# Kernel optimization log

Measured on AMD Instinct MI355X. Metric: run time of the kernel, lower is better.

The kernel has to match this reference:

```python
import jax, jax.numpy as jnp
import numpy as np

B, G, P, H = 32, 5000, 5000, 64
N = B * G
E_CO, E_GG = 1600000, 100000

def _bn(x, g, b):
    # BatchNorm1d in training mode: biased batch stats, eps=1e-5
    m = x.mean(0); v = x.var(0)
    return g * (x - m) * jax.lax.rsqrt(v + 1e-5) + b

def _renorm(t):
    # nn.Embedding(max_norm=True) -> rows renormed to L2 norm <= 1
    n = jnp.linalg.norm(t, axis=1, keepdims=True)
    return t * jnp.minimum(1.0, 1.0 / jnp.maximum(n, 1e-12))

def _sgconv(x, src, dst, w, W, b):
    # SGConv(K=1): gcn_norm (self-loops w=1, symmetric deg norm) spmm, then Linear
    n = x.shape[0]
    sl = jnp.arange(n)
    s = jnp.concatenate([src, sl]); d = jnp.concatenate([dst, sl])
    ww = jnp.concatenate([w, jnp.ones((n,), x.dtype)])
    deg = jax.ops.segment_sum(ww, d, num_segments=n)
    dinv = jnp.where(deg > 0, jax.lax.rsqrt(deg), 0.0)
    coef = dinv[s] * ww * dinv[d]
    agg = jax.ops.segment_sum(coef[:, None] * x[s], d, num_segments=n)
    return agg @ W.T + b

def _mlp3(x, W, b, g, bt):
    # MLP([h,h,h]): Lin-BN-ReLU-Lin-BN (trailing ReLU stripped by [:-1])
    h = jax.nn.relu(_bn(x @ W[0].T + b[0], g[0], bt[0]))
    return _bn(h @ W[1].T + b[1], g[1], bt[1])

def _gears(x, pert_idx, ei_co, w_co, ei_go, w_go, ei_bg, w_bg,
           gene_tab, pos_tab, go_tab, bg_tab, bn_g, bn_b, sg_W, sg_b,
           mlp_W, mlp_b, mlp_g, mlp_bt,
           rec_W1, rec_b1, rec_g1, rec_bt1, rec_W2, rec_b2, rec_g2, rec_bt2,
           indv_w1, indv_b1,
           cg_W1, cg_b1, cg_g1, cg_bt1, cg_W2, cg_b2, cg_g2, cg_bt2,
           indv_w2, indv_b2):
    nb = pert_idx.shape[0]
    ng = gene_tab.shape[0]
    emb = jnp.tile(_renorm(gene_tab), (nb, 1))                     # [B*G,H]
    base = jax.nn.relu(_bn(emb, bn_g[0], bn_b[0]))                 # bn_emb + emb_trans
    pos = jnp.tile(_renorm(pos_tab), (nb, 1))
    pos = _sgconv(pos, ei_co[0], ei_co[1], w_co, sg_W[0], sg_b[0]) # 1 gene-pos GNN layer, no trailing relu
    base = base + 0.2 * pos
    base = _mlp3(base, mlp_W[1], mlp_b[1], mlp_g[1], mlp_bt[1])    # emb_trans_v2
    pgo = _sgconv(_renorm(go_tab), ei_go[0], ei_go[1], w_go, sg_W[1], sg_b[1])
    pbg = _sgconv(_renorm(bg_tab), ei_bg[0], ei_bg[1], w_bg, sg_W[2], sg_b[2])
    pglob = _mlp3(pgo + pbg, mlp_W[0], mlp_b[0], mlp_g[0], mlp_bt[0])  # pert_emb_comb_trans
    base = base.reshape(nb, ng, -1)
    # one valid pert per graph -> pert_track reduces to a gather; pert_fuse then broadcast-add
    emb_total = _mlp3(pglob[pert_idx], mlp_W[2], mlp_b[2], mlp_g[2], mlp_bt[2])  # [B,H]
    base = base + emb_total[:, None, :]
    base = base.reshape(nb * ng, -1)
    base = jax.nn.relu(_bn(base, bn_g[1], bn_b[1]))                # bn_pert_base + transform
    h = jax.nn.relu(_bn(base @ rec_W1.T + rec_b1, rec_g1, rec_bt1))
    out = _bn(h @ rec_W2.T + rec_b2, rec_g2, rec_bt2).reshape(nb, ng, -1)
    w1 = jnp.einsum('bgh,gh->bg', out, indv_w1) + indv_b1          # per-gene decoder 1
    cg = jax.nn.relu(_bn(w1 @ cg_W1.T + cg_b1, cg_g1, cg_bt1))
    cg = _bn(cg @ cg_W2.T + cg_b2, cg_g2, cg_bt2)                  # cross_gene_state [B,H]
    cat = jnp.concatenate([w1[..., None], jnp.broadcast_to(cg[:, None, :], (nb, ng, cg.shape[-1]))], -1)
    out2 = jnp.einsum('bgk,gk->bg', cat, indv_w2) + indv_b2        # per-gene decoder 2
    return out2 + x.reshape(nb, ng)

def setup_inputs():
    ks = jax.random.split(jax.random.key(0), 48)
    rn = lambda i, sh, s=0.05: jax.random.normal(ks[i], sh, jnp.float32) * s
    return {
        "x": rn(0, (N,), 1.0),
        "pert_idx": jax.random.randint(ks[1], (B,), 0, P),
        "ei_co": jax.random.randint(ks[2], (2, E_CO), 0, N),
        "w_co": jax.random.uniform(ks[3], (E_CO,), jnp.float32),
        "ei_go": jax.random.randint(ks[4], (2, E_GG), 0, P),
        "w_go": jax.random.uniform(ks[5], (E_GG,), jnp.float32),
        "ei_bg": jax.random.randint(ks[6], (2, E_GG), 0, P),
        "w_bg": jax.random.uniform(ks[7], (E_GG,), jnp.float32),
        "gene_tab": rn(8, (G, H), 1.0),
        "pos_tab": rn(9, (G, H), 1.0),
        "go_tab": rn(10, (P, H), 1.0),
        "bg_tab": rn(11, (P, H), 1.0),
        "bn_g": jnp.ones((2, H)), "bn_b": jnp.zeros((2, H)),
        "sg_W": rn(12, (3, H, H)), "sg_b": jnp.zeros((3, H)),
        "mlp_W": rn(13, (3, 2, H, H)), "mlp_b": jnp.zeros((3, 2, H)),
        "mlp_g": jnp.ones((3, 2, H)), "mlp_bt": jnp.zeros((3, 2, H)),
        "rec_W1": rn(14, (2 * H, H)), "rec_b1": jnp.zeros((2 * H,)),
        "rec_g1": jnp.ones((2 * H,)), "rec_bt1": jnp.zeros((2 * H,)),
        "rec_W2": rn(15, (H, 2 * H)), "rec_b2": jnp.zeros((H,)),
        "rec_g2": jnp.ones((H,)), "rec_bt2": jnp.zeros((H,)),
        "indv_w1": rn(16, (G, H)), "indv_b1": rn(17, (G,)),
        "cg_W1": rn(18, (H, G), 0.01), "cg_b1": jnp.zeros((H,)),
        "cg_g1": jnp.ones((H,)), "cg_bt1": jnp.zeros((H,)),
        "cg_W2": rn(19, (H, H)), "cg_b2": jnp.zeros((H,)),
        "cg_g2": jnp.ones((H,)), "cg_bt2": jnp.zeros((H,)),
        "indv_w2": rn(20, (G, H + 1)), "indv_b2": rn(21, (G,)),
    }

def reference(x, pert_idx, ei_co, w_co, ei_go, w_go, ei_bg, w_bg,
              gene_tab, pos_tab, go_tab, bg_tab, bn_g, bn_b, sg_W, sg_b,
              mlp_W, mlp_b, mlp_g, mlp_bt,
              rec_W1, rec_b1, rec_g1, rec_bt1, rec_W2, rec_b2, rec_g2, rec_bt2,
              indv_w1, indv_b1,
              cg_W1, cg_b1, cg_g1, cg_bt1, cg_W2, cg_b2, cg_g2, cg_bt2,
              indv_w2, indv_b2):
    return _gears(x, pert_idx, ei_co, w_co, ei_go, w_go, ei_bg, w_bg,
                  gene_tab, pos_tab, go_tab, bg_tab, bn_g, bn_b, sg_W, sg_b,
                  mlp_W, mlp_b, mlp_g, mlp_bt,
                  rec_W1, rec_b1, rec_g1, rec_bt1, rec_W2, rec_b2, rec_g2, rec_bt2,
                  indv_w1, indv_b1,
                  cg_W1, cg_b1, cg_g1, cg_bt1, cg_W2, cg_b2, cg_g2, cg_bt2,
                  indv_w2, indv_b2)
```

## Files before the change

### kernel.cpp

```cpp
#include <hip/hip_runtime.h>

typedef unsigned int u32;
typedef unsigned short u16;

constexpr int Gn  = 5000;
constexpr int Bn  = 32;
constexpr int Pn  = 5000;
constexpr int Nn  = Bn * Gn;
constexpr int ECO = 1600000;
constexpr int EGG = 100000;
constexpr int NTILES = Nn / 128;
constexpr int PTILES = 40;
constexpr int NBK = 625;
constexpr int EPB2 = ECO / 256;

constexpr int oS2 = 128;
constexpr int oZERO = 1536;
constexpr int oA1 = 2048, oB1 = 2112, oA2 = 2176, oB2 = 2240;
constexpr int oA4 = 2304, oB4 = 2432;
constexpr int oA5 = 2560, oB5 = 2624;
constexpr int oAG = 2688, oBG = 2752;
constexpr int oAP1 = 2816, oBP1 = 2880, oAP2 = 2944, oBP2 = 3008;
constexpr int oAvec = 3072, oCvec = 3136, oCcP = 3200;
constexpr int oM  = 4096, oM1 = 8192;
constexpr int oE2 = 16384, oEMB = 18432, oCGRAW = 20480, oCG2 = 22528;
constexpr int oRG  = 24576;
constexpr int oRP  = oRG  + Gn * 64;
constexpr int oQ   = oRP  + Gn * 64;
constexpr int oRGO = oQ   + Gn * 64;
constexpr int oRBG = oRGO + Pn * 64;
constexpr int oAGO = oRBG + Pn * 64;
constexpr int oABG = oAGO + Pn * 64;
constexpr int oM1B = oABG + Pn * 64;
constexpr int oM2B = oM1B + Pn * 64;
constexpr int oDGO = oM2B + Pn * 64;
constexpr int oDBG = oDGO + Pn;
constexpr int oDEG = oDBG + Pn;
constexpr int oW1  = oDEG + Nn;
constexpr int oBUF0 = oW1 + Nn;
constexpr int oBUF1 = oBUF0 + Nn * 64;
constexpr size_t WS_FLOATS = (size_t)oBUF1 + (size_t)Nn * 64;

__device__ inline u16 f2bf(float f) {
  u32 u = __float_as_uint(f);
  u = (u + 0x7fffu + ((u >> 16) & 1u)) >> 16;
  return (u16)u;
}
__device__ inline float bflo(u32 v) { return __uint_as_float(v << 16); }
__device__ inline float bfhi(u32 v) { return __uint_as_float(v & 0xffff0000u); }
__device__ inline float bf2f(u16 v) { return __uint_as_float((u32)v << 16); }

typedef __attribute__((ext_vector_type(8))) short short8v;
typedef __attribute__((ext_vector_type(4))) float f32x4;

__global__ __launch_bounds__(256) void kzero(float* p, int n) {
  int i = blockIdx.x * 256 + threadIdx.x;
  if (i < n) p[i] = 0.f;
}

__global__ __launch_bounds__(256) void krenorm(const float* __restrict__ in, float* __restrict__ out,
                                               float* __restrict__ partial, u16* __restrict__ outb, int rows) {
  int lane = threadIdx.x & 63, wv = threadIdx.x >> 6;
  int gw = blockIdx.x * 4 + wv, nw = gridDim.x * 4;
  float ps = 0.f, pq = 0.f;
  for (int r = gw; r < rows; r += nw) {
    float v = in[r * 64 + lane];
    float sq = v * v;
    for (int off = 32; off; off >>= 1) sq += __shfl_xor(sq, off, 64);
    float nn = sqrtf(sq);
    float s = fminf(1.f, 1.f / fmaxf(nn, 1e-12f));
    float o = v * s;
    out[r * 64 + lane] = o;
    if (outb) outb[r * 64 + lane] = f2bf(o);
    ps += o; pq += o * o;
  }
  if (!partial) return;
  __shared__ float red[4][64], red2[4][64];
  red[wv][lane] = ps; red2[wv][lane] = pq;
  __syncthreads();
  if (wv == 0) {
    float s = red[0][lane] + red[1][lane] + red[2][lane] + red[3][lane];
    float q = red2[0][lane] + red2[1][lane] + red2[2][lane] + red2[3][lane];
    partial[blockIdx.x * 128 + lane] = s;
    partial[blockIdx.x * 128 + 64 + lane] = q;
  }
}

__global__ __launch_bounds__(1024) void kredfin(const float* __restrict__ part, int nblk, int outc,
                                                const float* __restrict__ g, const float* __restrict__ bt,
                                                float* __restrict__ a, float* __restrict__ b,
                                                float* __restrict__ outSQ, float invn) {
  __shared__ float rs[16][64], rq[16][64];
  int t = threadIdx.x, c = t & 63, seg = t >> 6;
  int col = blockIdx.x * 64 + c;
  int pitch = 2 * outc;
  float s = 0.f, q = 0.f;
  for (int r = seg; r < nblk; r += 16) {
    s += part[(size_t)r * pitch + col];
    q += part[(size_t)r * pitch + outc + col];
  }
  rs[seg][c] = s; rq[seg][c] = q;
  __syncthreads();
  if (t < 64) {
    int cc = blockIdx.x * 64 + t;
    float S = 0.f, Q = 0.f;
#pragma unroll
    for (int i = 0; i < 16; i++) { S += rs[i][t]; Q += rq[i][t]; }
    float mean = S * invn;
    float var = Q * invn - mean * mean;
    float sc = g[cc] * rsqrtf(var + 1e-5f);
    a[cc] = sc;
    b[cc] = bt[cc] - mean * sc;
    if (outSQ) { outSQ[cc] = S; outSQ[outc + cc] = Q; }
  }
}

__global__ __launch_bounds__(64) void kredB(const float* __restrict__ part, float* __restrict__ S3B) {
  int b = blockIdx.x;
  int c = threadIdx.x;
  float s = 0.f;
  int r0 = (b == 0) ? 0 : ((b - 1) * Gn) / 128;
  int r1 = ((b + 1) * Gn + 127) / 128;
  if (r1 > NTILES) r1 = NTILES;
  for (int r = r0; r < r1; r++) {
    int bLo = (r * 128) / Gn;
    if (bLo == b) s += part[(size_t)r * 128 + c];
    else if (bLo + 1 == b) s += part[(size_t)r * 128 + 64 + c];
  }
  S3B[b * 64 + c] = s;
}

__global__ __launch_bounds__(256) void ksmallmat(const float* __restrict__ A, const float* __restrict__ Bm,
                                                 float alpha, const float* __restrict__ bias,
                                                 const float* __restrict__ bv1, const float* __restrict__ bv2,
                                                 float beta, float* __restrict__ Mout, int mpitch,
                                                 float* __restrict__ cvec) {
  __shared__ float As[4096], Bs[4096];
  int t = threadIdx.x;
  for (int m = 0; m < 16; m++) { As[m * 256 + t] = A[m * 256 + t]; Bs[m * 256 + t] = Bm[m * 256 + t]; }
  __syncthreads();
  int j = t & 63, ig = t >> 6;
  for (int ii = 0; ii < 16; ii++) {
    int i = ig * 16 + ii;
    float acc = 0.f;
    for (int k = 0; k < 64; k++) acc += As[i * 64 + k] * Bs[k * 64 + j];
    Mout[i * mpitch + j] = alpha * acc;
  }
  if (cvec && t < 64) {
    float acc = bias ? bias[t] : 0.f;
    for (int k = 0; k < 64; k++) {
      float bb = (bv1 ? bv1[k] : 0.f) + (bv2 ? bv2[k] : 0.f);
      acc += beta * As[t * 64 + k] * bb;
    }
    cvec[t] = acc;
  }
}

__global__ __launch_bounds__(256) void khist(const int* __restrict__ dst, int* __restrict__ cnt,
                                             int* __restrict__ ticket, int E) {
  int e = blockIdx.x * 256 + threadIdx.x;
  if (e < E) ticket[e] = atomicAdd(&cnt[dst[e]], 1);
}

__global__ __launch_bounds__(256) void kscan1(const int* __restrict__ cnt, int* __restrict__ bsum, int n) {
  __shared__ int sh[256];
  int b = blockIdx.x, t = threadIdx.x;
  int base = b * 1024 + t * 4;
  int s = 0;
#pragma unroll
  for (int j = 0; j < 4; j++) { int i = base + j; if (i < n) s += cnt[i]; }
  sh[t] = s; __syncthreads();
  for (int d = 128; d; d >>= 1) { if (t < d) sh[t] += sh[t + d]; __syncthreads(); }
  if (t == 0) bsum[b] = sh[0];
}
__global__ __launch_bounds__(256) void kscan2(int* bsum, int nb, int* off_n) {
  __shared__ int sh[256];
  int t = threadIdx.x;
  int v = (t < nb) ? bsum[t] : 0;
  sh[t] = v;
  __syncthreads();
  for (int d = 1; d < 256; d <<= 1) {
    int u = (t >= d) ? sh[t - d] : 0;
    __syncthreads();
    sh[t] += u;
    __syncthreads();
// ... 73 lines not shown
  }
  int base = ssc[t] - s;
#pragma unroll
  for (int j = 0; j < 3; j++) {
    int i = i0 + j;
    if (i < NBK) { loff[i] = base; cur[i] = base; }
    base += c3[j];
  }
  __syncthreads();
  for (int e = e0 + t; e < e0 + EPB2; e += 256) {
    int d = dst[e];
    int pos = atomicAdd(&cur[d >> 8], 1);
    sbuf[pos] = make_float2(w[e], __int_as_float(src[e] | ((d & 255) << 18)));
  }
  __syncthreads();
  for (int i = t; i < EPB2; i += 256) stg[(size_t)e0 + i] = sbuf[i];
  for (int i = t; i < NBK; i += 256) {
    Cg[blockIdx.x * NBK + i] = cnt[i];
    Lg[blockIdx.x * NBK + i] = loff[i];
  }
}

__global__ __launch_bounds__(256) void ksumT(const int* __restrict__ Cg, int* __restrict__ T) {
  int bk = blockIdx.x * 256 + threadIdx.x;
  if (bk >= NBK) return;
  int s = 0;
  for (int blk = 0; blk < 256; blk++) s += Cg[blk * NBK + bk];
  T[bk] = s;
}

__global__ __launch_bounds__(256) void kpscan(const int* __restrict__ bcnt, int* __restrict__ bbase,
                                              int* __restrict__ offN) {
  __shared__ int sh[256];
  int t = threadIdx.x;
  int i0 = t * 3;
  int c[3];
  int s = 0;
#pragma unroll
  for (int j = 0; j < 3; j++) { int i = i0 + j; c[j] = (i < NBK) ? bcnt[i] : 0; s += c[j]; }
  sh[t] = s;
  __syncthreads();
  for (int d = 1; d < 256; d <<= 1) {
    int u = (t >= d) ? sh[t - d] : 0;
    __syncthreads();
    sh[t] += u;
    __syncthreads();
  }
  int base = sh[t] - s;
#pragma unroll
  for (int j = 0; j < 3; j++) {
    int i = i0 + j;
    if (i < NBK) bbase[i] = base;
    base += c[j];
  }
  if (t == 255) { bbase[NBK] = base; *offN = base; }
}

__global__ __launch_bounds__(256) void kpcsr2(const int* __restrict__ bbase, const int* __restrict__ Cg,
                                              const int* __restrict__ Lg, const float2* __restrict__ stg,
                                              int* __restrict__ off, float2* __restrict__ pack,
                                              float* __restrict__ dinv) {
  constexpr int CAP = 4096;
  __shared__ float2 ebuf[CAP];
  __shared__ int rh[256];
  __shared__ int sc2[256];
  __shared__ float ws[256];
  __shared__ int nEs;
  int bk = blockIdx.x, t = threadIdx.x;
  int myC = Cg[t * NBK + bk];
  int myL = Lg[t * NBK + bk];
  sc2[t] = myC;
  __syncthreads();
  for (int d = 1; d < 256; d <<= 1) {
    int u = (t >= d) ? sc2[t - d] : 0;
    __syncthreads();
    sc2[t] += u;
    __syncthreads();
  }
  int myO = sc2[t] - myC;
  if (t == 255) nEs = sc2[255];
  rh[t] = 0; ws[t] = 0.f;
  __syncthreads();
  int nE = nEs;
  {
    const float2* sp = &stg[(size_t)t * EPB2 + myL];
    for (int i = 0; i < myC; i++) ebuf[myO + i] = sp[i];
  }
  __syncthreads();
  for (int i = t; i < nE; i += 256) {
    float2 p = ebuf[i];
    int r = (__float_as_int(p.y) >> 18) & 255;
    atomicAdd(&rh[r], 1);
    atomicAdd(&ws[r], p.x);
  }
  __syncthreads();
  int cnt = rh[t];
  sc2[t] = cnt;
  __syncthreads();
  for (int d = 1; d < 256; d <<= 1) {
    int u = (t >= d) ? sc2[t - d] : 0;
    __syncthreads();
    sc2[t] += u;
    __syncthreads();
  }
  int gpos = bbase[bk] + sc2[t] - cnt;
  int grow = (bk << 8) + t;
  off[grow] = gpos;
  dinv[grow] = rsqrtf(1.f + ws[t]);
  rh[t] = gpos;
  __syncthreads();
  for (int i = t; i < nE; i += 256) {
    float2 p = ebuf[i];
    int r = (__float_as_int(p.y) >> 18) & 255;
    int pos = atomicAdd(&rh[r], 1);
    pack[pos] = p;
  }
}

__global__ __launch_bounds__(256) void kgather(const int* __restrict__ off, const float2* __restrict__ pack,
                                               const float* __restrict__ dinv, const float* __restrict__ tab,
                                               u16* __restrict__ aggb, int pitch, int coff, int n) {
  int lane = threadIdx.x & 63;
  int wv = blockIdx.x * 4 + (threadIdx.x >> 6);
  int nw = gridDim.x * 4;
  for (int i = wv; i < n; i += nw) {
    int b0 = off[i], b1 = off[i + 1];
    float di = dinv[i];
    float acc = di * tab[(i % Gn) * 64 + lane];
    for (int base = b0; base < b1; base += 64) {
      int m = b1 - base; if (m > 64) m = 64;
      float cj = 0.f; int idxj = 0;
      if (lane < m) {
        float2 p = pack[base + lane];
        int s = __float_as_int(p.y) & 0x3FFFF;
        cj = p.x * dinv[s];
        idxj = (s % Gn) * 64;
      }
      int j = 0;
      for (; j + 1 < m; j += 2) {
        float c0 = __shfl(cj, j, 64);     int i0 = __shfl(idxj, j, 64);
        float c1 = __shfl(cj, j + 1, 64); int i1 = __shfl(idxj, j + 1, 64);
        float t0 = tab[i0 + lane];
        float t1 = tab[i1 + lane];
        acc = fmaf(c0, t0, acc);
        acc = fmaf(c1, t1, acc);
      }
      if (j < m) {
        float c0 = __shfl(cj, j, 64); int i0 = __shfl(idxj, j, 64);
        acc = fmaf(c0, tab[i0 + lane], acc);
      }
    }
    acc *= di;
    aggb[(size_t)i * pitch + coff + lane] = f2bf(acc);
  }
}

template <int K, int OUTC, bool PRE, bool EB, bool PERG, bool STATS, bool OUTF32, bool STATB>
__global__ __launch_bounds__(256, 3) void mfgemm(
    const u16* __restrict__ Xb, const float* __restrict__ Wg, const float* __restrict__ bias,
    const float* __restrict__ pa, const float* __restrict__ pb,
    const float* __restrict__ perg, u16* __restrict__ Ybf, float* __restrict__ stats,
    float* __restrict__ statB, int rows) {
  constexpr int NT  = OUTC / 16;
  constexpr int KH  = K / 32;
  constexpr int SLK = K / 8;
  constexpr int SLO = OUTC / 8;
  constexpr int XROW = (K > OUTC ? K : OUTC) * 2;
  __shared__ __align__(16) unsigned char xsb[128 * XROW];
  __shared__ __align__(16) unsigned char wsb[OUTC * K * 2];
  __shared__ float sstat[STATS ? 2 * OUTC : 1];
  __shared__ float sstatB[STATB ? 128 : 1];
  int t = threadIdx.x;
  int l = t & 63, w = t >> 6, lrow = l & 15, lk = l >> 4;
  int R0 = blockIdx.x * 128;

  for (int idx = t; idx < OUTC * SLK; idx += 256) {
    int oc = idx / SLK, s8 = idx % SLK;
    const float* wp = &Wg[oc * K + s8 * 8];
    uint4 o;
    o.x = (u32)f2bf(wp[0]) | ((u32)f2bf(wp[1]) << 16);
    o.y = (u32)f2bf(wp[2]) | ((u32)f2bf(wp[3]) << 16);
    o.z = (u32)f2bf(wp[4]) | ((u32)f2bf(wp[5]) << 16);
    o.w = (u32)f2bf(wp[6]) | ((u32)f2bf(wp[7]) << 16);
    *(uint4*)&wsb[oc * (2 * K) + ((s8 * 16) ^ ((oc & 7) << 4))] = o;
  }
  if constexpr (STATS) for (int idx = t; idx < 2 * OUTC; idx += 256) sstat[idx] = 0.f;
  if constexpr (STATB) for (int idx = t; idx < 128; idx += 256) sstatB[idx] = 0.f;

#pragma unroll
  for (int m = 0; m < SLK / 2; m++) {
    int f = m * 256 + t;
    int r = f / SLK, s8 = f % SLK;
    uint4 u = *(const uint4*)&Xb[(size_t)(R0 + r) * K + s8 * 8];
    if constexpr (PRE) {
      int c0 = s8 * 8;
      float4 A0 = *(const float4*)&pa[c0];
      float4 A1 = *(const float4*)&pa[c0 + 4];
      const float* pbb = EB ? &pb[((R0 + r) / Gn) * 64] : pb;
      float4 B0 = *(const float4*)&pbb[c0];
      float4 B1 = *(const float4*)&pbb[c0 + 4];
      float v0 = fmaxf(fmaf(A0.x, bflo(u.x), B0.x), 0.f);
      float v1 = fmaxf(fmaf(A0.y, bfhi(u.x), B0.y), 0.f);
      float v2 = fmaxf(fmaf(A0.z, bflo(u.y), B0.z), 0.f);
      float v3 = fmaxf(fmaf(A0.w, bfhi(u.y), B0.w), 0.f);
      float v4 = fmaxf(fmaf(A1.x, bflo(u.z), B1.x), 0.f);
      float v5 = fmaxf(fmaf(A1.y, bfhi(u.z), B1.y), 0.f);
      float v6 = fmaxf(fmaf(A1.z, bflo(u.w), B1.z), 0.f);
      float v7 = fmaxf(fmaf(A1.w, bfhi(u.w), B1.w), 0.f);
      u.x = (u32)f2bf(v0) | ((u32)f2bf(v1) << 16);
      u.y = (u32)f2bf(v2) | ((u32)f2bf(v3) << 16);
      u.z = (u32)f2bf(v4) | ((u32)f2bf(v5) << 16);
      u.w = (u32)f2bf(v6) | ((u32)f2bf(v7) << 16);
    }
    *(uint4*)&xsb[r * XROW + ((s8 * 16) ^ ((r & 7) << 4))] = u;
  }
  float bcol[NT];
#pragma unroll
  for (int nt = 0; nt < NT; nt++) bcol[nt] = bias[nt * 16 + lrow];
  __syncthreads();

  short8v af[2][KH];
#pragma unroll
  for (int rt = 0; rt < 2; rt++)
#pragma unroll
    for (int h = 0; h < KH; h++) {
      int row = w * 32 + rt * 16 + lrow;
      af[rt][h] = *(const short8v*)&xsb[row * XROW + ((h * 64 + lk * 16) ^ ((row & 7) << 4))];
    }
  f32x4 acc[2][NT];
#pragma unroll
  for (int rt = 0; rt < 2; rt++)
#pragma unroll
    for (int nt = 0; nt < NT; nt++) {
      f32x4 z = {0.f, 0.f, 0.f, 0.f};
      acc[rt][nt] = z;
    }
#pragma unroll
  for (int nt = 0; nt < NT; nt++) {
    int brow = nt * 16 + lrow;
#pragma unroll
    for (int h = 0; h < KH; h++) {
      short8v bfr = *(const short8v*)&wsb[brow * (2 * K) + ((h * 64 + lk * 16) ^ ((brow & 7) << 4))];
      acc[0][nt] = __builtin_amdgcn_mfma_f32_16x16x32_bf16(af[0][h], bfr, acc[0][nt], 0, 0, 0);
      acc[1][nt] = __builtin_amdgcn_mfma_f32_16x16x32_bf16(af[1][h], bfr, acc[1][nt], 0, 0, 0);
    }
  }
  __syncthreads();

  float sS[NT], sQ[NT], sB0[NT], sB1[NT];
#pragma unroll
  for (int nt = 0; nt < NT; nt++) { sS[nt] = 0.f; sQ[nt] = 0.f; sB0[nt] = 0.f; sB1[nt] = 0.f; }
  int hiStart = STATB ? (R0 / Gn + 1) * Gn : 0x7fffffff;
  float* Yf = (float*)Ybf;
#pragma unroll
  for (int rt = 0; rt < 2; rt++) {
#pragma unroll
    for (int r = 0; r < 4; r++) {
      int orow = w * 32 + rt * 16 + lk * 4 + r;
      int grow = R0 + orow;
      bool valid = grow < rows;
      int qoff = 0;
      if constexpr (PERG) qoff = (grow % Gn) * 64;
#pragma unroll
      for (int nt = 0; nt < NT; nt++) {
        float v = acc[rt][nt][r] + bcol[nt];
        if constexpr (PERG) v += perg[qoff + nt * 16 + lrow];
        if (valid) {
          if constexpr (STATS) { sS[nt] += v; sQ[nt] += v * v; }
          if constexpr (STATB) { if (grow >= hiStart) sB1[nt] += v; else sB0[nt] += v; }
        }
        if constexpr (OUTF32) {
          if (valid) Yf[(size_t)grow * OUTC + nt * 16 + lrow] = v;
        } else {
          *(u16*)&xsb[orow * (2 * OUTC) + ((2 * (nt * 16 + lrow)) ^ ((orow & 7) << 4))] = f2bf(v);
        }
      }
    }
  }
  if constexpr (STATS) {
#pragma unroll
    for (int nt = 0; nt < NT; nt++) {
      atomicAdd(&sstat[nt * 16 + lrow], sS[nt]);
      atomicAdd(&sstat[OUTC + nt * 16 + lrow], sQ[nt]);
    }
  }
  if constexpr (STATB) {
#pragma unroll
    for (int nt = 0; nt < NT; nt++) {
      atomicAdd(&sstatB[nt * 16 + lrow], sB0[nt]);
      atomicAdd(&sstatB[64 + nt * 16 + lrow], sB1[nt]);
    }
  }
  __syncthreads();

  if constexpr (!OUTF32) {
#pragma unroll
    for (int m = 0; m < SLO / 2; m++) {
      int f = m * 256 + t;
      int r = f / SLO, c8 = f % SLO;
      uint4 o = *(const uint4*)&xsb[r * (2 * OUTC) + ((16 * c8) ^ ((r & 7) << 4))];
      *(uint4*)&Ybf[(size_t)(R0 + r) * OUTC + c8 * 8] = o;
    }
  }
  if constexpr (STATS)
    for (int idx = t; idx < 2 * OUTC; idx += 256) stats[(size_t)blockIdx.x * 2 * OUTC + idx] = sstat[idx];
  if constexpr (STATB)
    for (int idx = t; idx < 128; idx += 256) statB[(size_t)blockIdx.x * 128 + idx] = sstatB[idx];
// ... 125 lines not shown
    float a = b2[c];
    for (int k = 0; k < 64; k++) a += hmid[b * 64 + k] * W2[c * 64 + k];
    y[jb] = a; ps += a; pq += a * a;
  }
  sred[bg][c] = ps; qred[bg][c] = pq;
  __syncthreads();
  if (t < 64) {
    float s = sred[0][t] + sred[1][t] + sred[2][t] + sred[3][t];
    float q = qred[0][t] + qred[1][t] + qred[2][t] + qred[3][t];
    float mean = s * (1.f / 32.f), var = q * (1.f / 32.f) - mean * mean;
    float sc = g2[t] * rsqrtf(var + 1e-5f);
    asc[t] = sc; bsh[t] = bt2[t] - mean * sc;
  }
  __syncthreads();
  for (int jb = 0; jb < 8; jb++) { int b = bg * 8 + jb; cg2out[b * 64 + c] = asc[c] * y[jb] + bsh[c]; }
}

__global__ __launch_bounds__(256) void kemb(const u16* __restrict__ m2, const float* __restrict__ aP2,
                                            const float* __restrict__ bP2, const int* __restrict__ pidx,
                                            const float* __restrict__ Wm, const float* __restrict__ bv,
                                            const float* __restrict__ gg, const float* __restrict__ btv,
                                            float* __restrict__ emb) {
  int t = threadIdx.x, c = t & 63, bg = t >> 6;
  __shared__ float xin[2048], hmid[2048], sred[4][64], qred[4][64], asc[64], bsh[64];
  for (int idx = t; idx < 2048; idx += 256) {
    int b = idx >> 6, cc = idx & 63;
    xin[idx] = aP2[cc] * bf2f(m2[(size_t)pidx[b] * 64 + cc]) + bP2[cc];
  }
  __syncthreads();
  float y[8];
  float ps = 0.f, pq = 0.f;
  for (int jb = 0; jb < 8; jb++) {
    int b = bg * 8 + jb;
    float a = bv[c];
    for (int k = 0; k < 64; k++) a += xin[b * 64 + k] * Wm[c * 64 + k];
    y[jb] = a; ps += a; pq += a * a;
  }
  sred[bg][c] = ps; qred[bg][c] = pq;
  __syncthreads();
  if (t < 64) {
    float s = sred[0][t] + sred[1][t] + sred[2][t] + sred[3][t];
    float q = qred[0][t] + qred[1][t] + qred[2][t] + qred[3][t];
    float mean = s * (1.f / 32.f), var = q * (1.f / 32.f) - mean * mean;
    float sc = gg[t] * rsqrtf(var + 1e-5f);
    asc[t] = sc; bsh[t] = btv[t] - mean * sc;
  }
  __syncthreads();
  for (int jb = 0; jb < 8; jb++) { int b = bg * 8 + jb; hmid[b * 64 + c] = fmaxf(asc[c] * y[jb] + bsh[c], 0.f); }
  __syncthreads();
  ps = 0.f; pq = 0.f;
  for (int jb = 0; jb < 8; jb++) {
    int b = bg * 8 + jb;
    float a = bv[64 + c];
    for (int k = 0; k < 64; k++) a += hmid[b * 64 + k] * Wm[4096 + c * 64 + k];
    y[jb] = a; ps += a; pq += a * a;
  }
  sred[bg][c] = ps; qred[bg][c] = pq;
  __syncthreads();
  if (t < 64) {
    float s = sred[0][t] + sred[1][t] + sred[2][t] + sred[3][t];
    float q = qred[0][t] + qred[1][t] + qred[2][t] + qred[3][t];
    float mean = s * (1.f / 32.f), var = q * (1.f / 32.f) - mean * mean;
    float sc = gg[64 + t] * rsqrtf(var + 1e-5f);
    asc[t] = sc; bsh[t] = btv[64 + t] - mean * sc;
  }
  __syncthreads();
  for (int jb = 0; jb < 8; jb++) { int b = bg * 8 + jb; emb[b * 64 + c] = asc[c] * y[jb] + bsh[c]; }
}

__global__ __launch_bounds__(256) void kfinal(const float* __restrict__ w1, const float* __restrict__ cg2,
                                              const float* __restrict__ iw2, const float* __restrict__ ib2,
                                              const float* __restrict__ x, float* __restrict__ out) {
  __shared__ float iws[64 * 65], cgs[2048];
  int t = threadIdx.x;
  int g0 = blockIdx.x * 64;
  for (int idx = t; idx < 64 * 65; idx += 256) {
    int gi = g0 * 65 + idx;
    iws[idx] = (gi < Gn * 65) ? iw2[gi] : 0.f;
  }
  for (int idx = t; idx < 2048; idx += 256) cgs[idx] = cg2[idx];
  __syncthreads();
  int gl = t & 63, bg = t >> 6;
  int g = g0 + gl;
  if (g >= Gn) return;
  float bias = ib2[g];
  for (int jb = 0; jb < 8; jb++) {
    int b = bg * 8 + jb;
    float acc = w1[b * Gn + g] * iws[gl * 65] + bias;
    for (int k = 0; k < 64; k++) acc += cgs[b * 64 + k] * iws[gl * 65 + 1 + k];
    out[b * Gn + g] = acc + x[b * Gn + g];
  }
}

extern "C" void kernel_launch(void* const* d_in, const int* in_sizes, int n_in,
                              void* d_out, int out_size, void* d_ws, size_t ws_size,
                              hipStream_t stream) {
  (void)in_sizes; (void)n_in; (void)out_size;
  if (ws_size < WS_FLOATS * sizeof(float)) return;

  const float* x        = (const float*)d_in[0];
  const int*   pert_idx = (const int*)d_in[1];
  const int*   ei_co    = (const int*)d_in[2];
  const float* w_co     = (const float*)d_in[3];
  const int*   ei_go    = (const int*)d_in[4];
  const float* w_go     = (const float*)d_in[5];
  const int*   ei_bg    = (const int*)d_in[6];
  const float* w_bg     = (const float*)d_in[7];
  const float* gene_tab = (const float*)d_in[8];
  const float* pos_tab  = (const float*)d_in[9];
  const float* go_tab   = (const float*)d_in[10];
  const float* bg_tab   = (const float*)d_in[11];
  const float* bn_g     = (const float*)d_in[12];
  const float* bn_b     = (const float*)d_in[13];
  const float* sg_W     = (const float*)d_in[14];
  const float* sg_b     = (const float*)d_in[15];
  const float* mlp_W    = (const float*)d_in[16];
  const float* mlp_b    = (const float*)d_in[17];
  const float* mlp_g    = (const float*)d_in[18];
  const float* mlp_bt   = (const float*)d_in[19];
  const float* rec_W1   = (const float*)d_in[20];
  const float* rec_b1   = (const float*)d_in[21];
  const float* rec_g1   = (const float*)d_in[22];
  const float* rec_bt1  = (const float*)d_in[23];
  const float* rec_W2   = (const float*)d_in[24];
  const float* rec_b2   = (const float*)d_in[25];
  const float* rec_g2   = (const float*)d_in[26];
  const float* rec_bt2  = (const float*)d_in[27];
  const float* indv_w1  = (const float*)d_in[28];
  const float* indv_b1  = (const float*)d_in[29];
  const float* cg_W1    = (const float*)d_in[30];
  const float* cg_b1    = (const float*)d_in[31];
  const float* cg_g1    = (const float*)d_in[32];
  const float* cg_bt1   = (const float*)d_in[33];
  const float* cg_W2    = (const float*)d_in[34];
  const float* cg_b2    = (const float*)d_in[35];
  const float* cg_g2    = (const float*)d_in[36];
  const float* cg_bt2   = (const float*)d_in[37];
  const float* indv_w2  = (const float*)d_in[38];
  const float* indv_b2  = (const float*)d_in[39];

  float* W = (float*)d_ws;
  float* buf0 = W + oBUF0;
  float* buf1 = W + oBUF1;

  int*    co_off    = (int*)(buf1);
  int*    bbase     = (int*)(buf1 + 200000);
  int*    Tbk       = (int*)(buf1 + 202000);
  int*    sbsum     = (int*)(buf1 + 320128);
  float2* co_pack   = (float2*)(buf1 + 400000);
  int*    go_cnt    = (int*)(buf1 + 3700000);
  float2* go_pack   = (float2*)(buf1 + 3720000);
  int*    bg_cnt    = (int*)(buf1 + 4000000);
  float2* bg_pack   = (float2*)(buf1 + 4020000);
  int*    Cg        = (int*)(buf1 + 4500000);
  int*    Lg        = (int*)(buf1 + 4700000);
  int*    go_ticket = (int*)(buf1 + 6200000);
  int*    bg_ticket = (int*)(buf1 + 6400000);
  u16*    pgi       = (u16*)(buf1 + 6600000);
  u16*    RGB       = (u16*)(buf1 + 6800000);
  float2* co_stg    = (float2*)(buf1 + 6963840);

  float* partS = buf0 + 6000000;
  float* partB = buf0 + 6400000;

  kzero<<<8, 256, 0, stream>>>(W, 2048);
  kzero<<<15, 256, 0, stream>>>(buf1 + 6800000 + 160000, 3840);
  kzero<<<30, 256, 0, stream>>>(buf1 + 6600000 + 320000, 7680);
  krenorm<<<160, 256, 0, stream>>>(gene_tab, W + oRG, partS, RGB, Gn);
  kredfin<<<1, 1024, 0, stream>>>(partS, 160, 64, bn_g, bn_b, W + oAG, W + oBG, nullptr, 1.f / Gn);
  krenorm<<<160, 256, 0, stream>>>(pos_tab, W + oRP, nullptr, nullptr, Gn);
  krenorm<<<160, 256, 0, stream>>>(go_tab, W + oRGO, nullptr, nullptr, Pn);
  krenorm<<<160, 256, 0, stream>>>(bg_tab, W + oRBG, nullptr, nullptr, Pn);
  ksmallmat<<<1, 256, 0, stream>>>(mlp_W + 8192, sg_W, 0.2f, mlp_b + 128, sg_b, nullptr, 0.2f,
                                   W + oM, 64, W + oCvec);
  ksmallmat<<<1, 256, 0, stream>>>(mlp_W, sg_W + 4096, 1.f, nullptr, nullptr, nullptr, 0.f,
                                   W + oM1, 128, nullptr);
  ksmallmat<<<1, 256, 0, stream>>>(mlp_W, sg_W + 8192, 1.f, mlp_b, sg_b + 64, sg_b + 128, 1.f,
                                   W + oM1 + 64, 128, W + oCcP);
  mfgemm<64, 64, true, false, false, false, true, false><<<PTILES, 256, 0, stream>>>(
      RGB, mlp_W + 8192, W + oCvec, W + oAG, W + oBG, nullptr, (u16*)(W + oQ), nullptr, nullptr, Gn);

  kzero<<<(5001 + 255) / 256, 256, 0, stream>>>((float*)go_cnt, 5001);
  khist<<<(EGG + 255) / 256, 256, 0, stream>>>(ei_go + EGG, go_cnt, go_ticket, EGG);
  kscan1<<<5, 256, 0, stream>>>(go_cnt, sbsum, Pn);
  kscan2<<<1, 256, 0, stream>>>(sbsum, 5, go_cnt + Pn);
  kscan3<<<5, 256, 0, stream>>>(go_cnt, sbsum, Pn);
  kfillt<<<(EGG + 255) / 256, 256, 0, stream>>>(ei_go, ei_go + EGG, w_go, go_cnt, go_ticket, go_pack, EGG);
  kdinvrow<<<(Pn + 255) / 256, 256, 0, stream>>>(go_cnt, go_pack, W + oDGO, Pn);
  kgather<<<512, 256, 0, stream>>>(go_cnt, go_pack, W + oDGO, W + oRGO, pgi, 128, 0, Pn);

  kzero<<<(5001 + 255) / 256, 256, 0, stream>>>((float*)bg_cnt, 5001);
  khist<<<(EGG + 255) / 256, 256, 0, stream>>>(ei_bg + EGG, bg_cnt, bg_ticket, EGG);
  kscan1<<<5, 256, 0, stream>>>(bg_cnt, sbsum, Pn);
  kscan2<<<1, 256, 0, stream>>>(sbsum, 5, bg_cnt + Pn);
  kscan3<<<5, 256, 0, stream>>>(bg_cnt, sbsum, Pn);
  kfillt<<<(EGG + 255) / 256, 256, 0, stream>>>(ei_bg, ei_bg + EGG, w_bg, bg_cnt, bg_ticket, bg_pack, EGG);
  kdinvrow<<<(Pn + 255) / 256, 256, 0, stream>>>(bg_cnt, bg_pack, W + oDBG, Pn);
  kgather<<<512, 256, 0, stream>>>(bg_cnt, bg_pack, W + oDBG, W + oRBG, pgi, 128, 64, Pn);

  mfgemm<128, 64, false, false, false, true, false, false><<<PTILES, 256, 0, stream>>>(
      pgi, W + oM1, W + oCcP, nullptr, nullptr, nullptr, (u16*)(W + oM1B), partS, nullptr, Pn);
  kredfin<<<1, 1024, 0, stream>>>(partS, PTILES, 64, mlp_g, mlp_bt, W + oAP1, W + oBP1, nullptr, 1.f / Pn);
  mfgemm<64, 64, true, false, false, true, false, false><<<PTILES, 256, 0, stream>>>(
      (u16*)(W + oM1B), mlp_W + 4096, mlp_b + 64, W + oAP1, W + oBP1, nullptr,
      (u16*)(W + oM2B), partS, nullptr, Pn);
  kredfin<<<1, 1024, 0, stream>>>(partS, PTILES, 64, mlp_g + 64, mlp_bt + 64, W + oAP2, W + oBP2, nullptr, 1.f / Pn);
  kemb<<<1, 256, 0, stream>>>((u16*)(W + oM2B), W + oAP2, W + oBP2, pert_idx,
                              mlp_W + 16384, mlp_b + 256, mlp_g + 256, mlp_bt + 256, W + oEMB);

  kpsort<<<256, 256, 0, stream>>>(ei_co, ei_co + ECO, w_co, co_stg, Cg, Lg);
  ksumT<<<3, 256, 0, stream>>>(Cg, Tbk);
  kpscan<<<1, 256, 0, stream>>>(Tbk, bbase, co_off + Nn);
  kpcsr2<<<NBK, 256, 0, stream>>>(bbase, Cg, Lg, co_stg, co_off, co_pack, W + oDEG);
  kgather<<<2048, 256, 0, stream>>>(co_off, co_pack, W + oDEG, W + oRP, (u16*)buf0, 64, 0, Nn);

  mfgemm<64, 64, false, false, true, true, false, false><<<NTILES, 256, 0, stream>>>(
      (const u16*)buf0, W + oM, W + oZERO, nullptr, nullptr, W + oQ, (u16*)buf1, partS, nullptr, Nn);
  kredfin<<<1, 1024, 0, stream>>>(partS, NTILES, 64, mlp_g + 128, mlp_bt + 128, W + oA1, W + oB1, nullptr, 1.f / Nn);
  mfgemm<64, 64, true, false, false, true, false, true><<<NTILES, 256, 0, stream>>>(
      (const u16*)buf1, mlp_W + 12288, mlp_b + 192, W + oA1, W + oB1, nullptr,
      (u16*)buf0, partS, partB, Nn);
  kredfin<<<1, 1024, 0, stream>>>(partS, NTILES, 64, mlp_g + 192, mlp_bt + 192, W + oA2, W + oB2, W + oS2, 1.f / Nn);
  kredB<<<32, 64, 0, stream>>>(partB, W + oE2);
  kfinS3e2<<<1, 256, 0, stream>>>(W + oS2, bn_g + 64, bn_b + 64, W + oA2, W + oB2, W + oEMB,
                                  W + oE2, W + oAvec, W + oE2);
  mfgemm<64, 128, true, true, false, true, false, false><<<NTILES, 256, 0, stream>>>(
      (const u16*)buf0, rec_W1, rec_b1, W + oAvec, W + oE2, nullptr, (u16*)buf1, partS, nullptr, Nn);
  kredfin<<<2, 1024, 0, stream>>>(partS, NTILES, 128, rec_g1, rec_bt1, W + oA4, W + oB4, nullptr, 1.f / Nn);
  mfgemm<128, 64, true, false, false, true, false, false><<<NTILES, 256, 0, stream>>>(
      (const u16*)buf1, rec_W2, rec_b2, W + oA4, W + oB4, nullptr, (u16*)buf0, partS, nullptr, Nn);
  kredfin<<<1, 1024, 0, stream>>>(partS, NTILES, 64, rec_g2, rec_bt2, W + oA5, W + oB5, nullptr, 1.f / Nn);
  k13_kernel<<<(Nn * 16 + 255) / 256, 256, 0, stream>>>((const u16*)buf0, W + oA5, W + oB5, indv_w1, indv_b1,
                                                        W + oW1, Nn);
  kinitcg<<<8, 256, 0, stream>>>(cg_b1, W + oCGRAW);
  kcg1s<<<(Gn + 63) / 64, 256, 0, stream>>>(W + oW1, cg_W1, W + oCGRAW);
  kcg2<<<1, 256, 0, stream>>>(W + oCGRAW, cg_g1, cg_bt1, cg_W2, cg_b2, cg_g2, cg_bt2, W + oCG2);
  kfinal<<<(Gn + 63) / 64, 256, 0, stream>>>(W + oW1, W + oCG2, indv_w2, indv_b2, x, (float*)d_out);
}
```

Before: 735.7 us.

## Project position table before graph aggregation and fuse gather with batch stats

Uses linearity of the SGConv: the renormalized position table (5000 rows) is multiplied by the combined weight matrix once up front, and the 160k-row edge aggregation then gathers already-projected rows in fp32 float4 form. A new kernel kgt1 does the gather, self-loop term, Q add, bf16 store and per-block BN statistics together, which removes the full-size GEMM over 160k rows and one intermediate pass. In exchange the gather reads fp32 rows instead of bf16, and the per-block partial stats grow to 2048 blocks for kredfin. Buffers are swapped and partS is moved to avoid overlapping with the outputs.

```diff
diff --git a/kernel.cpp b/kernel.cpp
--- a/kernel.cpp
+++ b/kernel.cpp
@@ -29,8 +29,8 @@
 constexpr int oQ   = oRP  + Gn * 64;
 constexpr int oRGO = oQ   + Gn * 64;
 constexpr int oRBG = oRGO + Pn * 64;
-constexpr int oAGO = oRBG + Pn * 64;
-constexpr int oABG = oAGO + Pn * 64;
+constexpr int oPM  = oRBG + Pn * 64;
+constexpr int oABG = oPM + Pn * 64;
 constexpr int oM1B = oABG + Pn * 64;
 constexpr int oM2B = oM1B + Pn * 64;
 constexpr int oDGO = oM2B + Pn * 64;
@@ -410,6 +410,81 @@
     }
     acc *= di;
     aggb[(size_t)i * pitch + coff + lane] = f2bf(acc);
+  }
+}
+
+__global__ __launch_bounds__(256) void kgt1(const int* __restrict__ off, const float2* __restrict__ pack,
+                                            const float* __restrict__ dinv, const float4* __restrict__ PM4,
+                                            const float4* __restrict__ Q4, u16* __restrict__ Ybf,
+                                            float* __restrict__ partS) {
+  __shared__ float sred[4][64], sqred[4][64];
+  int t = threadIdx.x;
+  int lane = t & 63, wv = t >> 6;
+  int q = lane >> 4, kq = lane & 15;
+  int gw = blockIdx.x * 4 + wv, nw = gridDim.x * 4;
+  float4 sS = make_float4(0.f, 0.f, 0.f, 0.f);
+  float4 sQ = make_float4(0.f, 0.f, 0.f, 0.f);
+  for (int i = gw; i < Nn; i += nw) {
+    int g = i % Gn;
+    int b0 = off[i], b1 = off[i + 1];
+    float di = dinv[i];
+    float4 acc = make_float4(0.f, 0.f, 0.f, 0.f);
+    if (q == 0) {
+      float4 pm = PM4[g * 16 + kq];
+      acc.x = di * pm.x; acc.y = di * pm.y; acc.z = di * pm.z; acc.w = di * pm.w;
+    }
+    for (int base = b0; base < b1; base += 64) {
+      int m = b1 - base; if (m > 64) m = 64;
+      float cj = 0.f; int idx16 = 0;
+      if (lane < m) {
+        float2 p = pack[base + lane];
+        int s = __float_as_int(p.y) & 0x3FFFF;
+        cj = p.x * dinv[s];
+        idx16 = (s % Gn) * 16;
+      }
+      int steps = (m + 3) >> 2;
+      for (int st = 0; st < steps; st++) {
+        int e = st * 4 + q;
+        float c = __shfl(cj, e, 64);
+        int ix = __shfl(idx16, e, 64);
+        if (e < m) {
+          float4 tv = PM4[ix + kq];
+          acc.x = fmaf(c, tv.x, acc.x);
+          acc.y = fmaf(c, tv.y, acc.y);
+          acc.z = fmaf(c, tv.z, acc.z);
+          acc.w = fmaf(c, tv.w, acc.w);
+        }
+      }
+    }
+    acc.x += __shfl_xor(acc.x, 16, 64); acc.y += __shfl_xor(acc.y, 16, 64);
+    acc.z += __shfl_xor(acc.z, 16, 64); acc.w += __shfl_xor(acc.w, 16, 64);
+    acc.x += __shfl_xor(acc.x, 32, 64); acc.y += __shfl_xor(acc.y, 32, 64);
+    acc.z += __shfl_xor(acc.z, 32, 64); acc.w += __shfl_xor(acc.w, 32, 64);
+    float4 qv = Q4[g * 16 + kq];
+    float4 v;
+    v.x = fmaf(di, acc.x, qv.x); v.y = fmaf(di, acc.y, qv.y);
+    v.z = fmaf(di, acc.z, qv.z); v.w = fmaf(di, acc.w, qv.w);
+    if (q == 0) {
+      sS.x += v.x; sS.y += v.y; sS.z += v.z; sS.w += v.w;
+      sQ.x += v.x * v.x; sQ.y += v.y * v.y; sQ.z += v.z * v.z; sQ.w += v.w * v.w;
+      uint2 o;
+      o.x = (u32)f2bf(v.x) | ((u32)f2bf(v.y) << 16);
+      o.y = (u32)f2bf(v.z) | ((u32)f2bf(v.w) << 16);
+      *(uint2*)&Ybf[(size_t)i * 64 + kq * 4] = o;
+    }
+  }
+  if (q == 0) {
+    sred[wv][kq * 4 + 0] = sS.x; sred[wv][kq * 4 + 1] = sS.y;
+    sred[wv][kq * 4 + 2] = sS.z; sred[wv][kq * 4 + 3] = sS.w;
+    sqred[wv][kq * 4 + 0] = sQ.x; sqred[wv][kq * 4 + 1] = sQ.y;
+    sqred[wv][kq * 4 + 2] = sQ.z; sqred[wv][kq * 4 + 3] = sQ.w;
+  }
+  __syncthreads();
+  if (t < 64) {
+    float s = sred[0][t] + sred[1][t] + sred[2][t] + sred[3][t];
+    float qq = sqred[0][t] + sqred[1][t] + sqred[2][t] + sqred[3][t];
+    partS[(size_t)blockIdx.x * 128 + t] = s;
+    partS[(size_t)blockIdx.x * 128 + 64 + t] = qq;
   }
 }
 
@@ -842,6 +917,7 @@
   float2* go_pack   = (float2*)(buf1 + 3720000);
   int*    bg_cnt    = (int*)(buf1 + 4000000);
   float2* bg_pack   = (float2*)(buf1 + 4020000);
+  u16*    RPB       = (u16*)(buf1 + 4220000);
   int*    Cg        = (int*)(buf1 + 4500000);
   int*    Lg        = (int*)(buf1 + 4700000);
   int*    go_ticket = (int*)(buf1 + 6200000);
@@ -850,15 +926,16 @@
   u16*    RGB       = (u16*)(buf1 + 6800000);
   float2* co_stg    = (float2*)(buf1 + 6963840);
 
-  float* partS = buf0 + 6000000;
-  float* partB = buf0 + 6400000;
+  float* partS = buf1 + 8000000;
+  float* partB = buf1 + 8650000;
 
   kzero<<<8, 256, 0, stream>>>(W, 2048);
   kzero<<<15, 256, 0, stream>>>(buf1 + 6800000 + 160000, 3840);
+  kzero<<<15, 256, 0, stream>>>(buf1 + 4220000 + 160000, 3840);
   kzero<<<30, 256, 0, stream>>>(buf1 + 6600000 + 320000, 7680);
   krenorm<<<160, 256, 0, stream>>>(gene_tab, W + oRG, partS, RGB, Gn);
   kredfin<<<1, 1024, 0, stream>>>(partS, 160, 64, bn_g, bn_b, W + oAG, W + oBG, nullptr, 1.f / Gn);
-  krenorm<<<160, 256, 0, stream>>>(pos_tab, W + oRP, nullptr, nullptr, Gn);
+  krenorm<<<160, 256, 0, stream>>>(pos_tab, W + oRP, nullptr, RPB, Gn);
   krenorm<<<160, 256, 0, stream>>>(go_tab, W + oRGO, nullptr, nullptr, Pn);
   krenorm<<<160, 256, 0, stream>>>(bg_tab, W + oRBG, nullptr, nullptr, Pn);
   ksmallmat<<<1, 256, 0, stream>>>(mlp_W + 8192, sg_W, 0.2f, mlp_b + 128, sg_b, nullptr, 0.2f,
@@ -869,6 +946,8 @@
                                    W + oM1 + 64, 128, W + oCcP);
   mfgemm<64, 64, true, false, false, false, true, false><<<PTILES, 256, 0, stream>>>(
       RGB, mlp_W + 8192, W + oCvec, W + oAG, W + oBG, nullptr, (u16*)(W + oQ), nullptr, nullptr, Gn);
+  mfgemm<64, 64, false, false, false, false, true, false><<<PTILES, 256, 0, stream>>>(
+      RPB, W + oM, W + oZERO, nullptr, nullptr, nullptr, (u16*)(W + oPM), nullptr, nullptr, Gn);
 
   kzero<<<(5001 + 255) / 256, 256, 0, stream>>>((float*)go_cnt, 5001);
   khist<<<(EGG + 255) / 256, 256, 0, stream>>>(ei_go + EGG, go_cnt, go_ticket, EGG);
@@ -902,25 +981,25 @@
   ksumT<<<3, 256, 0, stream>>>(Cg, Tbk);
   kpscan<<<1, 256, 0, stream>>>(Tbk, bbase, co_off + Nn);
   kpcsr2<<<NBK, 256, 0, stream>>>(bbase, Cg, Lg, co_stg, co_off, co_pack, W + oDEG);
-  kgather<<<2048, 256, 0, stream>>>(co_off, co_pack, W + oDEG, W + oRP, (u16*)buf0, 64, 0, Nn);
-
-  mfgemm<64, 64, false, false, true, true, false, false><<<NTILES, 256, 0, stream>>>(
-      (const u16*)buf0, W + oM, W + oZERO, nullptr, nullptr, W + oQ, (u16*)buf1, partS, nullptr, Nn);
-  kredfin<<<1, 1024, 0, stream>>>(partS, NTILES, 64, mlp_g + 128, mlp_bt + 128, W + oA1, W + oB1, nullptr, 1.f / Nn);
+
+  kgt1<<<2048, 256, 0, stream>>>(co_off, co_pack, W + oDEG, (const float4*)(W + oPM),
+                                 (const float4*)(W + oQ), (u16*)buf0, partS);
+  kredfin<<<1, 1024, 0, stream>>>(partS, 2048, 64, mlp_g + 128, mlp_bt + 128, W + oA1, W + oB1, nullptr, 1.f / Nn);
+
   mfgemm<64, 64, true, false, false, true, false, true><<<NTILES, 256, 0, stream>>>(
-      (const u16*)buf1, mlp_W + 12288, mlp_b + 192, W + oA1, W + oB1, nullptr,
-      (u16*)buf0, partS, partB, Nn);
+      (const u16*)buf0, mlp_W + 12288, mlp_b + 192, W + oA1, W + oB1, nullptr,
+      (u16*)buf1, partS, partB, Nn);
   kredfin<<<1, 1024, 0, stream>>>(partS, NTILES, 64, mlp_g + 192, mlp_bt + 192, W + oA2, W + oB2, W + oS2, 1.f / Nn);
   kredB<<<32, 64, 0, stream>>>(partB, W + oE2);
   kfinS3e2<<<1, 256, 0, stream>>>(W + oS2, bn_g + 64, bn_b + 64, W + oA2, W + oB2, W + oEMB,
                                   W + oE2, W + oAvec, W + oE2);
   mfgemm<64, 128, true, true, false, true, false, false><<<NTILES, 256, 0, stream>>>(
-      (const u16*)buf0, rec_W1, rec_b1, W + oAvec, W + oE2, nullptr, (u16*)buf1, partS, nullptr, Nn);
+      (const u16*)buf1, rec_W1, rec_b1, W + oAvec, W + oE2, nullptr, (u16*)buf0, partS, nullptr, Nn);
   kredfin<<<2, 1024, 0, stream>>>(partS, NTILES, 128, rec_g1, rec_bt1, W + oA4, W + oB4, nullptr, 1.f / Nn);
   mfgemm<128, 64, true, false, false, true, false, false><<<NTILES, 256, 0, stream>>>(
-      (const u16*)buf1, rec_W2, rec_b2, W + oA4, W + oB4, nullptr, (u16*)buf0, partS, nullptr, Nn);
+      (const u16*)buf0, rec_W2, rec_b2, W + oA4, W + oB4, nullptr, (u16*)buf1, partS, nullptr, Nn);
   kredfin<<<1, 1024, 0, stream>>>(partS, NTILES, 64, rec_g2, rec_bt2, W + oA5, W + oB5, nullptr, 1.f / Nn);
-  k13_kernel<<<(Nn * 16 + 255) / 256, 256, 0, stream>>>((const u16*)buf0, W + oA5, W + oB5, indv_w1, indv_b1,
+  k13_kernel<<<(Nn * 16 + 255) / 256, 256, 0, stream>>>((const u16*)buf1, W + oA5, W + oB5, indv_w1, indv_b1,
                                                         W + oW1, Nn);
   kinitcg<<<8, 256, 0, stream>>>(cg_b1, W + oCGRAW);
   kcg1s<<<(Gn + 63) / 64, 256, 0, stream>>>(W + oW1, cg_W1, W + oCGRAW);
```

Result: slower. 791.5 us (+7.6%).

## Premultiply pos table by folded weight, fuse co-expression gather with BN stats

Applied to the files above, without the earlier changes.

Uses linearity of the SGConv: the renormed pos table (5000 rows) is multiplied by the folded weight matrix once, up front. The per-node gather then aggregates these pre-transformed 64-wide bf16 rows, adds the per-gene Q term and accumulates batch-norm statistics in the same pass. This removes the full Nn-row GEMM and one round trip of the intermediate through memory. In exchange, the gather now works on already-projected bf16 values, which may shift rounding, and the stats reduction runs over 2048 partial blocks instead of NTILES.

```diff
diff --git a/kernel.cpp b/kernel.cpp
--- a/kernel.cpp
+++ b/kernel.cpp
@@ -29,8 +29,8 @@
 constexpr int oQ   = oRP  + Gn * 64;
 constexpr int oRGO = oQ   + Gn * 64;
 constexpr int oRBG = oRGO + Pn * 64;
-constexpr int oAGO = oRBG + Pn * 64;
-constexpr int oABG = oAGO + Pn * 64;
+constexpr int oPM  = oRBG + Pn * 64;
+constexpr int oABG = oPM + Pn * 64;
 constexpr int oM1B = oABG + Pn * 64;
 constexpr int oM2B = oM1B + Pn * 64;
 constexpr int oDGO = oM2B + Pn * 64;
@@ -411,6 +411,85 @@
     acc *= di;
     aggb[(size_t)i * pitch + coff + lane] = f2bf(acc);
   }
+}
+
+__global__ __launch_bounds__(256) void kgt2(const int* __restrict__ off, const float2* __restrict__ pack,
+                                            const float* __restrict__ dinv, const uint4* __restrict__ PMB,
+                                            const float4* __restrict__ Q4, u16* __restrict__ Ybf,
+                                            float* __restrict__ partS) {
+  __shared__ float sstat[128];
+  int t = threadIdx.x;
+  int lane = t & 63, wv = t >> 6;
+  int grp = lane >> 3, le = lane & 7;
+  for (int idx = t; idx < 128; idx += 256) sstat[idx] = 0.f;
+  __syncthreads();
+  float sS[8], sQ[8];
+#pragma unroll
+  for (int j = 0; j < 8; j++) { sS[j] = 0.f; sQ[j] = 0.f; }
+  int base0 = (blockIdx.x * 4 + wv) * 8;
+  int stride = gridDim.x * 32;
+  for (int i0 = base0; i0 < Nn; i0 += stride) {
+    int i = i0 + grp;
+    int g = i % Gn;
+    int b0 = off[i], b1 = off[i + 1];
+    float di = dinv[i];
+    float acc[8];
+    {
+      uint4 tv = PMB[g * 8 + le];
+      acc[0] = di * bflo(tv.x); acc[1] = di * bfhi(tv.x);
+      acc[2] = di * bflo(tv.y); acc[3] = di * bfhi(tv.y);
+      acc[4] = di * bflo(tv.z); acc[5] = di * bfhi(tv.z);
+      acc[6] = di * bflo(tv.w); acc[7] = di * bfhi(tv.w);
+    }
+    for (int base = b0; base < b1; base += 8) {
+      int m = b1 - base; if (m > 8) m = 8;
+      float cj = 0.f; int ix = 0;
+      if (le < m) {
+        float2 p = pack[base + le];
+        int s = __float_as_int(p.y) & 0x3FFFF;
+        cj = p.x * dinv[s];
+        ix = s % Gn;
+      }
+#pragma unroll
+      for (int e = 0; e < 8; e++) {
+        float c = __shfl(cj, grp * 8 + e, 64);
+        int x = __shfl(ix, grp * 8 + e, 64);
+        if (e < m) {
+          uint4 tv = PMB[x * 8 + le];
+          acc[0] = fmaf(c, bflo(tv.x), acc[0]);
+          acc[1] = fmaf(c, bfhi(tv.x), acc[1]);
+          acc[2] = fmaf(c, bflo(tv.y), acc[2]);
+          acc[3] = fmaf(c, bfhi(tv.y), acc[3]);
+          acc[4] = fmaf(c, bflo(tv.z), acc[4]);
+          acc[5] = fmaf(c, bfhi(tv.z), acc[5]);
+          acc[6] = fmaf(c, bflo(tv.w), acc[6]);
+          acc[7] = fmaf(c, bfhi(tv.w), acc[7]);
+        }
+      }
+    }
+    float4 q0 = Q4[g * 16 + le * 2];
+    float4 q1 = Q4[g * 16 + le * 2 + 1];
+    float v[8];
+    v[0] = fmaf(di, acc[0], q0.x); v[1] = fmaf(di, acc[1], q0.y);
+    v[2] = fmaf(di, acc[2], q0.z); v[3] = fmaf(di, acc[3], q0.w);
+    v[4] = fmaf(di, acc[4], q1.x); v[5] = fmaf(di, acc[5], q1.y);
+    v[6] = fmaf(di, acc[6], q1.z); v[7] = fmaf(di, acc[7], q1.w);
+#pragma unroll
+    for (int j = 0; j < 8; j++) { sS[j] += v[j]; sQ[j] += v[j] * v[j]; }
+    uint4 o;
+    o.x = (u32)f2bf(v[0]) | ((u32)f2bf(v[1]) << 16);
+    o.y = (u32)f2bf(v[2]) | ((u32)f2bf(v[3]) << 16);
+    o.z = (u32)f2bf(v[4]) | ((u32)f2bf(v[5]) << 16);
+    o.w = (u32)f2bf(v[6]) | ((u32)f2bf(v[7]) << 16);
+    *(uint4*)&Ybf[(size_t)i * 64 + le * 8] = o;
+  }
+#pragma unroll
+  for (int j = 0; j < 8; j++) {
+    atomicAdd(&sstat[le * 8 + j], sS[j]);
+    atomicAdd(&sstat[64 + le * 8 + j], sQ[j]);
+  }
+  __syncthreads();
+  for (int idx = t; idx < 128; idx += 256) partS[(size_t)blockIdx.x * 128 + idx] = sstat[idx];
 }
 
 template <int K, int OUTC, bool PRE, bool EB, bool PERG, bool STATS, bool OUTF32, bool STATB>
@@ -842,6 +921,7 @@
   float2* go_pack   = (float2*)(buf1 + 3720000);
   int*    bg_cnt    = (int*)(buf1 + 4000000);
   float2* bg_pack   = (float2*)(buf1 + 4020000);
+  u16*    RPB       = (u16*)(buf1 + 4220000);
   int*    Cg        = (int*)(buf1 + 4500000);
   int*    Lg        = (int*)(buf1 + 4700000);
   int*    go_ticket = (int*)(buf1 + 6200000);
@@ -850,15 +930,16 @@
   u16*    RGB       = (u16*)(buf1 + 6800000);
   float2* co_stg    = (float2*)(buf1 + 6963840);
 
-  float* partS = buf0 + 6000000;
-  float* partB = buf0 + 6400000;
+  float* partS = buf1 + 8000000;
+  float* partB = buf1 + 8650000;
 
   kzero<<<8, 256, 0, stream>>>(W, 2048);
   kzero<<<15, 256, 0, stream>>>(buf1 + 6800000 + 160000, 3840);
+  kzero<<<15, 256, 0, stream>>>(buf1 + 4220000 + 160000, 3840);
   kzero<<<30, 256, 0, stream>>>(buf1 + 6600000 + 320000, 7680);
   krenorm<<<160, 256, 0, stream>>>(gene_tab, W + oRG, partS, RGB, Gn);
   kredfin<<<1, 1024, 0, stream>>>(partS, 160, 64, bn_g, bn_b, W + oAG, W + oBG, nullptr, 1.f / Gn);
-  krenorm<<<160, 256, 0, stream>>>(pos_tab, W + oRP, nullptr, nullptr, Gn);
+  krenorm<<<160, 256, 0, stream>>>(pos_tab, W + oRP, nullptr, RPB, Gn);
   krenorm<<<160, 256, 0, stream>>>(go_tab, W + oRGO, nullptr, nullptr, Pn);
   krenorm<<<160, 256, 0, stream>>>(bg_tab, W + oRBG, nullptr, nullptr, Pn);
   ksmallmat<<<1, 256, 0, stream>>>(mlp_W + 8192, sg_W, 0.2f, mlp_b + 128, sg_b, nullptr, 0.2f,
@@ -869,6 +950,8 @@
                                    W + oM1 + 64, 128, W + oCcP);
   mfgemm<64, 64, true, false, false, false, true, false><<<PTILES, 256, 0, stream>>>(
       RGB, mlp_W + 8192, W + oCvec, W + oAG, W + oBG, nullptr, (u16*)(W + oQ), nullptr, nullptr, Gn);
+  mfgemm<64, 64, false, false, false, false, false, false><<<PTILES, 256, 0, stream>>>(
+      RPB, W + oM, W + oZERO, nullptr, nullptr, nullptr, (u16*)(W + oPM), nullptr, nullptr, Gn);
 
   kzero<<<(5001 + 255) / 256, 256, 0, stream>>>((float*)go_cnt, 5001);
   khist<<<(EGG + 255) / 256, 256, 0, stream>>>(ei_go + EGG, go_cnt, go_ticket, EGG);
@@ -902,25 +985,25 @@
   ksumT<<<3, 256, 0, stream>>>(Cg, Tbk);
   kpscan<<<1, 256, 0, stream>>>(Tbk, bbase, co_off + Nn);
   kpcsr2<<<NBK, 256, 0, stream>>>(bbase, Cg, Lg, co_stg, co_off, co_pack, W + oDEG);
-  kgather<<<2048, 256, 0, stream>>>(co_off, co_pack, W + oDEG, W + oRP, (u16*)buf0, 64, 0, Nn);
-
-  mfgemm<64, 64, false, false, true, true, false, false><<<NTILES, 256, 0, stream>>>(
-      (const u16*)buf0, W + oM, W + oZERO, nullptr, nullptr, W + oQ, (u16*)buf1, partS, nullptr, Nn);
-  kredfin<<<1, 1024, 0, stream>>>(partS, NTILES, 64, mlp_g + 128, mlp_bt + 128, W + oA1, W + oB1, nullptr, 1.f / Nn);
+
+  kgt2<<<2048, 256, 0, stream>>>(co_off, co_pack, W + oDEG, (const uint4*)(W + oPM),
+                                 (const float4*)(W + oQ), (u16*)buf0, partS);
+  kredfin<<<1, 1024, 0, stream>>>(partS, 2048, 64, mlp_g + 128, mlp_bt + 128, W + oA1, W + oB1, nullptr, 1.f / Nn);
+
   mfgemm<64, 64, true, false, false, true, false, true><<<NTILES, 256, 0, stream>>>(
-      (const u16*)buf1, mlp_W + 12288, mlp_b + 192, W + oA1, W + oB1, nullptr,
-      (u16*)buf0, partS, partB, Nn);
+      (const u16*)buf0, mlp_W + 12288, mlp_b + 192, W + oA1, W + oB1, nullptr,
+      (u16*)buf1, partS, partB, Nn);
   kredfin<<<1, 1024, 0, stream>>>(partS, NTILES, 64, mlp_g + 192, mlp_bt + 192, W + oA2, W + oB2, W + oS2, 1.f / Nn);
   kredB<<<32, 64, 0, stream>>>(partB, W + oE2);
   kfinS3e2<<<1, 256, 0, stream>>>(W + oS2, bn_g + 64, bn_b + 64, W + oA2, W + oB2, W + oEMB,
                                   W + oE2, W + oAvec, W + oE2);
   mfgemm<64, 128, true, true, false, true, false, false><<<NTILES, 256, 0, stream>>>(
-      (const u16*)buf0, rec_W1, rec_b1, W + oAvec, W + oE2, nullptr, (u16*)buf1, partS, nullptr, Nn);
+      (const u16*)buf1, rec_W1, rec_b1, W + oAvec, W + oE2, nullptr, (u16*)buf0, partS, nullptr, Nn);
   kredfin<<<2, 1024, 0, stream>>>(partS, NTILES, 128, rec_g1, rec_bt1, W + oA4, W + oB4, nullptr, 1.f / Nn);
   mfgemm<128, 64, true, false, false, true, false, false><<<NTILES, 256, 0, stream>>>(
-      (const u16*)buf1, rec_W2, rec_b2, W + oA4, W + oB4, nullptr, (u16*)buf0, partS, nullptr, Nn);
+      (const u16*)buf0, rec_W2, rec_b2, W + oA4, W + oB4, nullptr, (u16*)buf1, partS, nullptr, Nn);
   kredfin<<<1, 1024, 0, stream>>>(partS, NTILES, 64, rec_g2, rec_bt2, W + oA5, W + oB5, nullptr, 1.f / Nn);
-  k13_kernel<<<(Nn * 16 + 255) / 256, 256, 0, stream>>>((const u16*)buf0, W + oA5, W + oB5, indv_w1, indv_b1,
+  k13_kernel<<<(Nn * 16 + 255) / 256, 256, 0, stream>>>((const u16*)buf1, W + oA5, W + oB5, indv_w1, indv_b1,
                                                         W + oW1, Nn);
   kinitcg<<<8, 256, 0, stream>>>(cg_b1, W + oCGRAW);
   kcg1s<<<(Gn + 63) / 64, 256, 0, stream>>>(W + oW1, cg_W1, W + oCGRAW);
```

Measured after the change: 751.0 us. +2.1%, slower.
